# Kernel tuning notes

Hardware: AMD Instinct MI355X
Metric: run time of the kernel (lower is better)

## Reference

```python
import jax, jax.numpy as jnp
import numpy as np

B, S, D, H = 2, 2048, 1024, 16
DK = D // H

def setup_inputs() -> dict:
    key = jax.random.key(0)
    ks = jax.random.split(key, 5)
    scale = 1.0 / np.sqrt(D)
    return {
        "query": jax.random.normal(ks[0], (B, S, D), dtype=jnp.float32),
        "mask": jnp.ones((B, S, S), dtype=jnp.int32),
        "Wq": jax.random.normal(ks[1], (D, D), dtype=jnp.float32) * scale,
        "bq": jnp.zeros((D,), dtype=jnp.float32),
        "Wk": jax.random.normal(ks[2], (D, D), dtype=jnp.float32) * scale,
        "bk": jnp.zeros((D,), dtype=jnp.float32),
        "Wv": jax.random.normal(ks[3], (D, D), dtype=jnp.float32) * scale,
        "bv": jnp.zeros((D,), dtype=jnp.float32),
        "Wo": jax.random.normal(ks[4], (D, D), dtype=jnp.float32) * scale,
        "bo": jnp.zeros((D,), dtype=jnp.float32),
    }

def reference(query, mask, Wq, bq, Wk, bk, Wv, bv, Wo, bo):
    # self-attention: key = value = query (torch Linear: x @ W.T + b)
    b, s, d = query.shape
    def proj(x, W, bias):
        y = jnp.einsum('bsd,ed->bse', x, W) + bias
        return y.reshape(b, s, H, DK).transpose(0, 2, 1, 3)  # [B,H,S,DK]
    q = proj(query, Wq, bq)
    k = proj(query, Wk, bk)
    v = proj(query, Wv, bv)
    scores = jnp.einsum('bhqd,bhkd->bhqk', q, k) / jnp.sqrt(jnp.float32(DK))
    m = mask[:, None, :, :]  # [B,1,S,S] (torch unsqueeze(1) for 3D mask)
    scores = jnp.where(m == 0, jnp.float32(-1e9), scores)
    w = jax.nn.softmax(scores, axis=-1)  # dropout: eval mode -> identity
    o = jnp.einsum('bhqk,bhkd->bhqd', w, v)
    o = o.transpose(0, 2, 1, 3).reshape(b, s, d)
    return jnp.einsum('bsd,ed->bse', o, Wo) + bo
```

## Files before the change

### kernel.cpp

```cpp
#include <hip/hip_runtime.h>


typedef _Float16 f16x8 __attribute__((ext_vector_type(8)));
typedef _Float16 f16x4 __attribute__((ext_vector_type(4)));
typedef _Float16 f16x2 __attribute__((ext_vector_type(2)));
typedef float    f32x4 __attribute__((ext_vector_type(4)));
typedef float    f32x16 __attribute__((ext_vector_type(16)));
typedef int      i32x4 __attribute__((ext_vector_type(4)));
typedef unsigned u32x2 __attribute__((ext_vector_type(2)));

#define MFMA32(a, b, c) __builtin_amdgcn_mfma_f32_32x32x16_f16(a, b, c, 0, 0, 0)
#define MFMA16(a, b, c) __builtin_amdgcn_mfma_f32_16x16x32_f16(a, b, c, 0, 0, 0)

#if __has_builtin(__builtin_amdgcn_exp2f)
#define EXP2(x) __builtin_amdgcn_exp2f(x)
#else
#define EXP2(x) exp2f(x)
#endif

__device__ __forceinline__ void gld16(const void* g, void* l) {
    __builtin_amdgcn_global_load_lds(
        (const __attribute__((address_space(1))) void*)g,
        (__attribute__((address_space(3))) void*)l, 16, 0, 0);
}

__device__ __forceinline__ void conv1k(const float* __restrict__ in,
                                       _Float16* __restrict__ out, int base) {
    const int i = base + threadIdx.x * 4;
    float4 v = *(const float4*)(in + i);
    f16x4 o;
    o.x = (_Float16)v.x; o.y = (_Float16)v.y; o.z = (_Float16)v.z; o.w = (_Float16)v.w;
    *(f16x4*)(out + i) = o;
}

__global__ void k_pre(const float* __restrict__ X, const float* __restrict__ Wq,
                      const float* __restrict__ Wk, const float* __restrict__ Wv,
                      const float* __restrict__ Wo,
                      _Float16* __restrict__ Xh, _Float16* __restrict__ Wqh,
                      _Float16* __restrict__ Wkh, _Float16* __restrict__ Wvh,
                      _Float16* __restrict__ Woh,
                      const int* __restrict__ mask, int* __restrict__ flag) {
    const int bid = blockIdx.x;
    if (bid < 4096)      conv1k(X,  Xh,  bid * 1024);
    else if (bid < 5120) conv1k(Wq, Wqh, (bid - 4096) * 1024);
    else if (bid < 6144) conv1k(Wk, Wkh, (bid - 5120) * 1024);
    else if (bid < 7168) conv1k(Wv, Wvh, (bid - 6144) * 1024);
    else if (bid < 8192) conv1k(Wo, Woh, (bid - 7168) * 1024);
    else {
        const int i = (bid - 8192) * 1024 + threadIdx.x * 4;
        int4 v = *(const int4*)(mask + i);
        if ((v.x == 0) | (v.y == 0) | (v.z == 0) | (v.w == 0)) atomicOr(flag, 1);
    }
}

__global__ __launch_bounds__(256, 3) void k_qkv(
    const _Float16* __restrict__ X,
    const _Float16* __restrict__ Wqh, const _Float16* __restrict__ Wkh,
    const _Float16* __restrict__ Wvh,
    const float* __restrict__ bq, const float* __restrict__ bk,
    const float* __restrict__ bv,
    _Float16* __restrict__ Qo, _Float16* __restrict__ Ko, _Float16* __restrict__ Vo)
{
    __shared__ _Float16 SH[128 * 136];
    _Float16* As = SH;
    _Float16* Bs = SH + 128 * 64;
    const int tid = threadIdx.x;
    const int lane = tid & 63, wv = tid >> 6;
    const int wrow = wv >> 1, wcol = wv & 1;
    const int l5 = lane & 31, half = lane >> 5;
    const int which = blockIdx.x >> 3;
    const _Float16* W   = which == 0 ? Wqh : which == 1 ? Wkh : Wvh;
    const float*   bias = which == 0 ? bq  : which == 1 ? bk  : bv;
    const int n0 = (blockIdx.x & 7) * 128;
    const int m0 = blockIdx.y * 128;

    f32x16 acc[2][2];
#pragma unroll
    for (int a = 0; a < 2; ++a)
#pragma unroll
        for (int bb = 0; bb < 2; ++bb)
#pragma unroll
            for (int r = 0; r < 16; ++r) acc[a][bb][r] = 0.f;

#pragma unroll 1
    for (int k0 = 0; k0 < 1024; k0 += 64) {
        __syncthreads();
#pragma unroll
        for (int it = 0; it < 4; ++it) {
            const int wbase = it * 256 + wv * 64;
            const int ci = wbase + lane;
            const int r = ci >> 3;
            const int c8 = (((ci & 7) ^ (r & 7)) * 8);
            gld16(X + (size_t)(m0 + r) * 1024 + k0 + c8, As + wbase * 8);
            gld16(W + (size_t)(n0 + r) * 1024 + k0 + c8, Bs + wbase * 8);
        }
        __syncthreads();
#pragma unroll
        for (int ks = 0; ks < 4; ++ks) {
            f16x8 af[2], bf[2];
#pragma unroll
            for (int mt = 0; mt < 2; ++mt)
                af[mt] = *(const f16x8*)(As + (wrow * 64 + mt * 32 + l5) * 64 +
                                         (((ks * 2 + half) ^ (l5 & 7)) * 8));
#pragma unroll
            for (int nt = 0; nt < 2; ++nt)
                bf[nt] = *(const f16x8*)(Bs + (wcol * 64 + nt * 32 + l5) * 64 +
                                         (((ks * 2 + half) ^ (l5 & 7)) * 8));
#pragma unroll
            for (int mt = 0; mt < 2; ++mt)
#pragma unroll
                for (int nt = 0; nt < 2; ++nt)
                    acc[mt][nt] = MFMA32(af[mt], bf[nt], acc[mt][nt]);
        }
    }

    __syncthreads();
    const int b_ = m0 >> 11;
    const int s_base = m0 & 2047;
    if (which == 2) {
#pragma unroll
        for (int nt = 0; nt < 2; ++nt) {
            const int e_l = wcol * 64 + nt * 32 + l5;
            const float bv_ = bias[n0 + e_l];
#pragma unroll
            for (int mt = 0; mt < 2; ++mt)
#pragma unroll
                for (int g = 0; g < 4; ++g) {
                    const int m_l = wrow * 64 + mt * 32 + 8 * g + 4 * half;
                    f16x4 pk;
#pragma unroll
                    for (int j = 0; j < 4; ++j)
                        pk[j] = (_Float16)(acc[mt][nt][4 * g + j] + bv_);
                    *(f16x4*)(SH + e_l * 136 + m_l) = pk;
                }
        }
        __syncthreads();
#pragma unroll
        for (int p = 0; p < 8; ++p) {
            const int e_l = p * 16 + (tid >> 4);
            const int s8 = (tid & 15) * 8;
            f16x8 vv = *(const f16x8*)(SH + e_l * 136 + s8);
            const int e = n0 + e_l;
            const int h = e >> 6, dk = e & 63;
            const int s0 = s_base + s8;
            const size_t idx = ((((size_t)(b_ * 16 + h) * 128 + (s0 >> 4)) * 2 +
                                (dk >> 5)) * 64 + (dk & 31) + 32 * ((s8 >> 3) & 1)) * 8;
            *(f16x8*)(Vo + idx) = vv;
        }
    } else {
        const float qs = (which == 0) ? 0.18033688011112042f : 1.0f;
#pragma unroll
        for (int nt = 0; nt < 2; ++nt) {
            const int e_l = wcol * 64 + nt * 32 + l5;
            const float bv_ = bias[n0 + e_l];
#pragma unroll
            for (int mt = 0; mt < 2; ++mt)
#pragma unroll
                for (int r = 0; r < 16; ++r) {
                    const int m_l = wrow * 64 + mt * 32 + (r & 3) + 8 * (r >> 2) + 4 * half;
                    SH[m_l * 136 + e_l] = (_Float16)((acc[mt][nt][r] + bv_) * qs);
                }
        }
        __syncthreads();
#pragma unroll
        for (int p = 0; p < 8; ++p) {
            const int m_l = p * 16 + (tid >> 4);
            const int c8 = (tid & 15) * 8;
            f16x8 vv = *(const f16x8*)(SH + m_l * 136 + c8);
            const int e = n0 + c8;
            const int h = e >> 6, dk = e & 63;
            const int s = s_base + m_l;
            if (which == 0) {
                *(f16x8*)(Qo + (((size_t)b_ * 16 + h) * 2048 + s) * 64 + dk) = vv;
            } else {
                const size_t idx = ((((size_t)(b_ * 16 + h) * 64 + (s >> 5)) * 4 +
                                    (dk >> 4)) * 64 + (s & 31) + 32 * ((dk >> 3) & 1)) * 8;
                *(f16x8*)(Ko + idx) = vv;
            }
        }
    }
}

__global__ __launch_bounds__(256, 4) void k_oproj(
    const _Float16* __restrict__ Oin, const _Float16* __restrict__ Woh,
    const float* __restrict__ bo, float* __restrict__ out)
{
    __shared__ _Float16 As[128 * 64];
    __shared__ _Float16 Bs[64 * 64];
    const int tid = threadIdx.x;
    const int lane = tid & 63, wv = tid >> 6;
    const int quad = lane >> 4, lc = lane & 15;
    const int n0 = blockIdx.x * 64;
    const int m0 = blockIdx.y * 128;

    const f32x4 fzero = {0.f, 0.f, 0.f, 0.f};
    f32x4 acc[2][4];
#pragma unroll
    for (int a = 0; a < 2; ++a)
#pragma unroll
        for (int bb = 0; bb < 4; ++bb) acc[a][bb] = fzero;

#pragma unroll 1
    for (int k0 = 0; k0 < 1024; k0 += 64) {
        __syncthreads();
#pragma unroll
        for (int it = 0; it < 4; ++it) {
            const int ci = it * 256 + tid;
            const int r = ci >> 3;
            const int c8 = (((ci & 7) ^ (r & 7)) * 8);
            gld16(Oin + (size_t)(m0 + r) * 1024 + k0 + c8, As + ci * 8);
        }
#pragma unroll
        for (int it = 0; it < 2; ++it) {
            const int ci = it * 256 + tid;
            const int r = ci >> 3;
            const int c8 = (((ci & 7) ^ (r & 7)) * 8);
            gld16(Woh + (size_t)(n0 + r) * 1024 + k0 + c8, Bs + ci * 8);
        }
        __syncthreads();
#pragma unroll
        for (int ks = 0; ks < 2; ++ks) {
            f16x8 af[2], bf[4];
#pragma unroll
            for (int mt = 0; mt < 2; ++mt)
                af[mt] = *(const f16x8*)(As + (wv * 32 + mt * 16 + lc) * 64 +
                                         (((ks * 4 + quad) ^ (lc & 7)) * 8));
#pragma unroll
            for (int nt = 0; nt < 4; ++nt)
                bf[nt] = *(const f16x8*)(Bs + (nt * 16 + lc) * 64 +
                                         (((ks * 4 + quad) ^ (lc & 7)) * 8));
#pragma unroll
            for (int mt = 0; mt < 2; ++mt)
#pragma unroll
                for (int nt = 0; nt < 4; ++nt)
                    acc[mt][nt] = MFMA16(af[mt], bf[nt], acc[mt][nt]);
        }
    }
#pragma unroll
    for (int nt = 0; nt < 4; ++nt) {
        const int e = n0 + nt * 16 + lc;
        const float bv_ = bo[e];
#pragma unroll
        for (int mt = 0; mt < 2; ++mt)
#pragma unroll
            for (int i = 0; i < 4; ++i) {
                const int m = m0 + wv * 32 + mt * 16 + quad * 4 + i;
                out[(size_t)m * 1024 + e] = acc[mt][nt][i] + bv_;
            }
    }
}

__global__ __launch_bounds__(256, 4) void k_attn(
    const _Float16* __restrict__ Q, const _Float16* __restrict__ Kp,
    const _Float16* __restrict__ Vp, const int* __restrict__ mask,
    const int* __restrict__ flag, _Float16* __restrict__ O)
{
    __shared__ float Os[2][32 * 64];
    __shared__ float Ls[2][32];

    const int tid = threadIdx.x;
    const int lane = tid & 63, wv = tid >> 6;
    const int l5 = lane & 31, half = lane >> 5;
    const int qt = wv >> 1, kh = wv & 1;
    const int bh = blockIdx.x;
    const int b = bh >> 4, h = bh & 15;
    const int qb = blockIdx.y * 64 + qt * 32;
    const int phase = (bh & 3) * 8;

    const _Float16* Qb = Q  + (size_t)bh * 2048 * 64;
    const _Float16* Kb = Kp + (size_t)bh * 131072;
    const _Float16* Vb = Vp + (size_t)bh * 131072;

    f16x8 qf[4];
#pragma unroll
    for (int kk = 0; kk < 4; ++kk)
        qf[kk] = *(const f16x8*)(Qb + (size_t)(qb + l5) * 64 + kk * 16 + half * 8);

    const f16x2 one2 = {(_Float16)1.f, (_Float16)1.f};

    f32x16 o[2];
#pragma unroll
    for (int nt = 0; nt < 2; ++nt)
#pragma unroll
        for (int r = 0; r < 16; ++r) o[nt][r] = 0.f;
    float l_i = 0.f;

    const bool has_zero = (*flag != 0);

    f16x8 kf[4];
    {
        const int kb0 = kh * 32 + phase;
#pragma unroll
        for (int kk = 0; kk < 4; ++kk)
            kf[kk] = *(const f16x8*)(Kb + ((size_t)(kb0 * 4 + kk) * 64 + lane) * 8);
    }

#pragma unroll 2
    for (int it = 0; it < 32; ++it) {
        const int kb = kh * 32 + ((it + phase) & 31);
        f16x8 vf[4];
#pragma unroll
        for (int ks = 0; ks < 2; ++ks)
#pragma unroll
            for (int nt = 0; nt < 2; ++nt)
                vf[ks * 2 + nt] = *(const f16x8*)(Vb +
                    ((size_t)((kb * 2 + ks) * 2 + nt) * 64 + lane) * 8);

        f32x16 st;
#pragma unroll
        for (int r = 0; r < 16; ++r) st[r] = 0.f;
        __builtin_amdgcn_s_setprio(1);
        st = MFMA32(kf[0], qf[0], st);
        st = MFMA32(kf[1], qf[1], st);
        st = MFMA32(kf[2], qf[2], st);
        st = MFMA32(kf[3], qf[3], st);
        __builtin_amdgcn_s_setprio(0);

        {
            const int nkb = kh * 32 + ((it + 1 + phase) & 31);
#pragma unroll
            for (int kk = 0; kk < 4; ++kk)
                kf[kk] = *(const f16x8*)(Kb + ((size_t)(nkb * 4 + kk) * 64 + lane) * 8);
        }

        if (has_zero) {
            const int q = qb + l5;
            const int* mr = mask + ((size_t)b * 2048 + q) * 2048 + kb * 32;
            for (int r = 0; r < 16; ++r) {
                const int kk_ = (r & 3) + 8 * (r >> 2) + 4 * half;
                if (mr[kk_] == 0) st[r] = -1e30f;
            }
        }

        unsigned u[8];
        float rs = 0.f;
#pragma unroll
        for (int j = 0; j < 8; ++j) {
            const float p0 = EXP2(st[2 * j]);
            const float p1 = EXP2(st[2 * j + 1]);
            u[j] = __builtin_bit_cast(unsigned, __builtin_amdgcn_cvt_pkrtz(p0, p1));
#if __has_builtin(__builtin_amdgcn_fdot2)
            rs = __builtin_amdgcn_fdot2(__builtin_bit_cast(f16x2, u[j]), one2, rs, false);
#else
            rs += p0 + p1;
#endif
        }
        rs += __shfl_xor(rs, 32);
        l_i += rs;

        u32x2 r02 = __builtin_amdgcn_permlane32_swap(u[0], u[2], false, false);
        u32x2 r13 = __builtin_amdgcn_permlane32_swap(u[1], u[3], false, false);
        u32x2 r46 = __builtin_amdgcn_permlane32_swap(u[4], u[6], false, false);
        u32x2 r57 = __builtin_amdgcn_permlane32_swap(u[5], u[7], false, false);
        i32x4 a0 = { (int)r02[0], (int)r13[0], (int)r02[1], (int)r13[1] };
        i32x4 a1 = { (int)r46[0], (int)r57[0], (int)r46[1], (int)r57[1] };
        f16x8 pa0 = __builtin_bit_cast(f16x8, a0);
        f16x8 pa1 = __builtin_bit_cast(f16x8, a1);

        __builtin_amdgcn_s_setprio(1);
        o[0] = MFMA32(pa0, vf[0], o[0]);
        o[1] = MFMA32(pa0, vf[1], o[1]);
        o[0] = MFMA32(pa1, vf[2], o[0]);
        o[1] = MFMA32(pa1, vf[3], o[1]);
        __builtin_amdgcn_s_setprio(0);
    }

    if (kh == 1) {
        if (half == 0) Ls[qt][l5] = l_i;
#pragma unroll
        for (int nt = 0; nt < 2; ++nt)
#pragma unroll
            for (int r = 0; r < 16; ++r) {
                const int q_loc = (r & 3) + 8 * (r >> 2) + 4 * half;
                Os[qt][q_loc * 64 + nt * 32 + l5] = o[nt][r];
            }
    }
    __syncthreads();
    if (kh == 0) {
        const float linv = 1.f / (l_i + Ls[qt][l5]);
#pragma unroll
        for (int r = 0; r < 16; ++r) {
            const int q_loc = (r & 3) + 8 * (r >> 2) + 4 * half;
            const float lv = __shfl(linv, q_loc);
            const int q = qb + q_loc;
            _Float16* orow = O + ((size_t)b * 2048 + q) * 1024 + h * 64;
#pragma unroll
            for (int nt = 0; nt < 2; ++nt) {
                const float val = o[nt][r] + Os[qt][q_loc * 64 + nt * 32 + l5];
                orow[nt * 32 + l5] = (_Float16)(val * lv);
            }
        }
    }
}

extern "C" void kernel_launch(void* const* d_in, const int* in_sizes, int n_in,
                              void* d_out, int out_size, void* d_ws, size_t ws_size,
                              hipStream_t stream) {
    const float* query = (const float*)d_in[0];
    const int*   mask  = (const int*)d_in[1];
    const float* Wq = (const float*)d_in[2]; const float* bq = (const float*)d_in[3];
    const float* Wk = (const float*)d_in[4]; const float* bk = (const float*)d_in[5];
    const float* Wv = (const float*)d_in[6]; const float* bv = (const float*)d_in[7];
    const float* Wo = (const float*)d_in[8]; const float* bo = (const float*)d_in[9];
    float* out = (float*)d_out;

    char* ws = (char*)d_ws;
    _Float16* Xh  = (_Float16*)(ws);
    _Float16* Wqh = (_Float16*)(ws + 8388608);
    _Float16* Wkh = (_Float16*)(ws + 10485760);
    _Float16* Wvh = (_Float16*)(ws + 12582912);
    _Float16* Woh = (_Float16*)(ws + 14680064);
    _Float16* Qh  = (_Float16*)(ws + 16777216);
    _Float16* Kh  = (_Float16*)(ws + 25165824);
    _Float16* Vh  = (_Float16*)(ws + 33554432);
    _Float16* Oh  = Xh;
    int* flag     = (int*)(ws + 41943040);

    (void)hipMemsetAsync(flag, 0, 4, stream);
    k_pre<<<16384, 256, 0, stream>>>(query, Wq, Wk, Wv, Wo,
                                     Xh, Wqh, Wkh, Wvh, Woh, mask, flag);
    k_qkv<<<dim3(24, 32), 256, 0, stream>>>(Xh, Wqh, Wkh, Wvh, bq, bk, bv, Qh, Kh, Vh);
    k_attn<<<dim3(32, 32), 256, 0, stream>>>(Qh, Kh, Vh, mask, flag, Oh);
    k_oproj<<<dim3(16, 32), 256, 0, stream>>>(Oh, Woh, bo, out);
}
```

Measured before the change: 208.9 us.

## Move mask scan into QKV GEMM grid and drop memset

The mask all-ones check moves out of the conversion kernel and into extra blocks of the QKV projection launch, so the 32 MB mask read can run alongside the GEMM tiles. The flag is now cleared inside k_pre instead of by a separate memset launch. This removes one launch and takes the mask read off the conversion kernel's critical path. The cost is extra blocks competing with the GEMM blocks for bandwidth and CU slots. The flag must also be set before k_attn reads it, which stream order guarantees.

```diff
diff --git a/kernel.cpp b/kernel.cpp
--- a/kernel.cpp
+++ b/kernel.cpp
@@ -38,19 +38,14 @@
                       const float* __restrict__ Wo,
                       _Float16* __restrict__ Xh, _Float16* __restrict__ Wqh,
                       _Float16* __restrict__ Wkh, _Float16* __restrict__ Wvh,
-                      _Float16* __restrict__ Woh,
-                      const int* __restrict__ mask, int* __restrict__ flag) {
+                      _Float16* __restrict__ Woh, int* __restrict__ flag) {
     const int bid = blockIdx.x;
+    if (bid == 0 && threadIdx.x == 0) *flag = 0;
     if (bid < 4096)      conv1k(X,  Xh,  bid * 1024);
     else if (bid < 5120) conv1k(Wq, Wqh, (bid - 4096) * 1024);
     else if (bid < 6144) conv1k(Wk, Wkh, (bid - 5120) * 1024);
     else if (bid < 7168) conv1k(Wv, Wvh, (bid - 6144) * 1024);
-    else if (bid < 8192) conv1k(Wo, Woh, (bid - 7168) * 1024);
-    else {
-        const int i = (bid - 8192) * 1024 + threadIdx.x * 4;
-        int4 v = *(const int4*)(mask + i);
-        if ((v.x == 0) | (v.y == 0) | (v.z == 0) | (v.w == 0)) atomicOr(flag, 1);
-    }
+    else                 conv1k(Wo, Woh, (bid - 7168) * 1024);
 }
 
 __global__ __launch_bounds__(256, 3) void k_qkv(
@@ -59,12 +54,27 @@
     const _Float16* __restrict__ Wvh,
     const float* __restrict__ bq, const float* __restrict__ bk,
     const float* __restrict__ bv,
-    _Float16* __restrict__ Qo, _Float16* __restrict__ Ko, _Float16* __restrict__ Vo)
+    _Float16* __restrict__ Qo, _Float16* __restrict__ Ko, _Float16* __restrict__ Vo,
+    const int* __restrict__ mask, int* __restrict__ flag)
 {
     __shared__ _Float16 SH[128 * 136];
+    const int tid = threadIdx.x;
+
+    if (blockIdx.x >= 24) {
+        const int sb = (blockIdx.x - 24) + 8 * blockIdx.y;
+        const int4* m4 = (const int4*)mask + (size_t)sb * 8192 + tid;
+        int bad = 0;
+#pragma unroll 4
+        for (int i = 0; i < 32; ++i) {
+            int4 v = m4[i * 256];
+            bad |= (v.x == 0) | (v.y == 0) | (v.z == 0) | (v.w == 0);
+        }
+        if (bad) atomicOr(flag, 1);
+        return;
+    }
+
     _Float16* As = SH;
     _Float16* Bs = SH + 128 * 64;
-    const int tid = threadIdx.x;
     const int lane = tid & 63, wv = tid >> 6;
     const int wrow = wv >> 1, wcol = wv & 1;
     const int l5 = lane & 31, half = lane >> 5;
@@ -416,10 +426,10 @@
     _Float16* Oh  = Xh;
     int* flag     = (int*)(ws + 41943040);
 
-    (void)hipMemsetAsync(flag, 0, 4, stream);
-    k_pre<<<16384, 256, 0, stream>>>(query, Wq, Wk, Wv, Wo,
-                                     Xh, Wqh, Wkh, Wvh, Woh, mask, flag);
-    k_qkv<<<dim3(24, 32), 256, 0, stream>>>(Xh, Wqh, Wkh, Wvh, bq, bk, bv, Qh, Kh, Vh);
+    k_pre<<<8192, 256, 0, stream>>>(query, Wq, Wk, Wv, Wo,
+                                    Xh, Wqh, Wkh, Wvh, Woh, flag);
+    k_qkv<<<dim3(32, 32), 256, 0, stream>>>(Xh, Wqh, Wkh, Wvh, bq, bk, bv,
+                                            Qh, Kh, Vh, mask, flag);
     k_attn<<<dim3(32, 32), 256, 0, stream>>>(Qh, Kh, Vh, mask, flag, Oh);
     k_oproj<<<dim3(16, 32), 256, 0, stream>>>(Oh, Woh, bo, out);
 }
```

New measurement: 207.7 us (median of 2 runs). Within noise of the previous version (-0.6%).
